# Performance work log

Measured on AMD Instinct MI355X. Metric: run time of the kernel, lower is better.

The kernel has to match this reference:

```python
import jax, jax.numpy as jnp
import numpy as np
import math

D_MODEL = 512
NUM_HEADS = 8
HEAD_DIM = D_MODEL // NUM_HEADS
B, S = 4, 2048


def setup_inputs() -> dict:
    key = jax.random.key(0)
    ks = jax.random.split(key, 11)
    scale = 1.0 / math.sqrt(D_MODEL)
    inp = {
        "Q": jax.random.normal(ks[0], (B, S, D_MODEL), jnp.float32),
        "K": jax.random.normal(ks[1], (B, S, D_MODEL), jnp.float32),
        "V": jax.random.normal(ks[2], (B, S, D_MODEL), jnp.float32),
        # causal mask, broadcast over batch and heads: [1,1,S,S]
        "mask": jnp.tril(jnp.ones((S, S), dtype=bool))[None, None],
        "w_q": jax.random.normal(ks[3], (D_MODEL, D_MODEL), jnp.float32) * scale,
        "b_q": jnp.zeros((D_MODEL,), jnp.float32),
        "w_k": jax.random.normal(ks[4], (D_MODEL, D_MODEL), jnp.float32) * scale,
        "b_k": jnp.zeros((D_MODEL,), jnp.float32),
        "w_v": jax.random.normal(ks[5], (D_MODEL, D_MODEL), jnp.float32) * scale,
        "b_v": jnp.zeros((D_MODEL,), jnp.float32),
        "w_o": jax.random.normal(ks[6], (D_MODEL, D_MODEL), jnp.float32) * scale,
        "b_o": jnp.zeros((D_MODEL,), jnp.float32),
    }
    return inp


def _split_heads(x):
    b, s, _ = x.shape
    return x.reshape(b, s, NUM_HEADS, HEAD_DIM).transpose(0, 2, 1, 3)  # [B,H,S,Dh]


def reference(Q, K, V, mask, w_q, b_q, w_k, b_k, w_v, b_v, w_o, b_o):
    # Linear projections (torch Linear: x @ W.T + b)
    q = _split_heads(Q @ w_q.T + b_q)
    k = _split_heads(K @ w_k.T + b_k)
    v = _split_heads(V @ w_v.T + b_v)

    scores = jnp.einsum("bhqd,bhkd->bhqk", q, k) / math.sqrt(HEAD_DIM)
    scores = jnp.where(mask, scores, -jnp.inf)
    attention = jax.nn.softmax(scores, axis=-1)  # [B,H,S,S]
    ctx = jnp.einsum("bhqk,bhkd->bhqd", attention, v)

    b, h, s, dh = ctx.shape
    x = ctx.transpose(0, 2, 1, 3).reshape(b, s, D_MODEL)
    x = x @ w_o.T + b_o
    return (x, attention)
```

## Files before the change

### kernel.cpp

```cpp
#include <hip/hip_runtime.h>


#define BATCH 4
#define SEQ   2048
#define DM    512
#define NH    8
#define DH    64
#define ROWS  (BATCH*SEQ)
#define QT    (SEQ/64)

typedef unsigned short u16;
using bf8   = __attribute__((ext_vector_type(8))) short;
using f32x4 = __attribute__((ext_vector_type(4))) float;

__device__ __forceinline__ float b2f(u16 u) {
    union { unsigned int i; float f; } v; v.i = ((unsigned int)u) << 16; return v.f;
}
__device__ __forceinline__ u16 f2b(float f) {
    union { float fl; unsigned int i; } v; v.fl = f;
    return (u16)((v.i + 0x7FFFu + ((v.i >> 16) & 1u)) >> 16);
}

template<bool IN_BF16, bool OUT_BF16>
__global__ __launch_bounds__(256) void proj_mfma(
    const void* __restrict__ Xv, const float* __restrict__ W,
    const float* __restrict__ bias, void* __restrict__ Cv)
{
    __shared__ u16 Xs[128][40];
    __shared__ u16 Wsh[128][40];
    const int tid  = threadIdx.x;
    const int lane = tid & 63;
    const int w    = tid >> 6;
    const int wm = (w >> 1) * 64, wn = (w & 1) * 64;
    const int lc = lane & 15, lq = lane >> 4;
    const int row0 = blockIdx.y * 128;
    const int col0 = blockIdx.x * 128;

    const f32x4 fzero = {0.f, 0.f, 0.f, 0.f};
    f32x4 acc[4][4];
    #pragma unroll
    for (int mt = 0; mt < 4; ++mt)
        #pragma unroll
        for (int nt = 0; nt < 4; ++nt) acc[mt][nt] = fzero;

    for (int k0 = 0; k0 < DM; k0 += 32) {
        __syncthreads();
        if (IN_BF16) {
            const u16* Xg = (const u16*)Xv;
            const int r = tid >> 2, kc = (tid & 3) * 8;
            #pragma unroll
            for (int rr = 0; rr < 2; ++rr)
                *(bf8*)&Xs[r + rr*64][kc] =
                    *(const bf8*)(Xg + (size_t)(row0 + r + rr*64) * DM + k0 + kc);
        } else {
            const float* Xg = (const float*)Xv;
            const int r = tid >> 3, kc = (tid & 7) * 4;
            #pragma unroll
            for (int rr = 0; rr < 4; ++rr) {
                float4 vx = *(const float4*)(Xg + (size_t)(row0 + r + rr*32) * DM + k0 + kc);
                u16 t4[4] = { f2b(vx.x), f2b(vx.y), f2b(vx.z), f2b(vx.w) };
                *(uint2*)&Xs[r + rr*32][kc] = *(uint2*)t4;
            }
        }
        {
            const int r = tid >> 3, kc = (tid & 7) * 4;
            #pragma unroll
            for (int rr = 0; rr < 4; ++rr) {
                float4 vw = *(const float4*)(W + (size_t)(col0 + r + rr*32) * DM + k0 + kc);
                u16 t4[4] = { f2b(vw.x), f2b(vw.y), f2b(vw.z), f2b(vw.w) };
                *(uint2*)&Wsh[r + rr*32][kc] = *(uint2*)t4;
            }
        }
        __syncthreads();
        bf8 a[4], b[4];
        #pragma unroll
        for (int mt = 0; mt < 4; ++mt) a[mt] = *(const bf8*)&Xs[wm + mt*16 + lc][lq*8];
        #pragma unroll
        for (int nt = 0; nt < 4; ++nt) b[nt] = *(const bf8*)&Wsh[wn + nt*16 + lc][lq*8];
        #pragma unroll
        for (int mt = 0; mt < 4; ++mt)
            #pragma unroll
            for (int nt = 0; nt < 4; ++nt)
                acc[mt][nt] = __builtin_amdgcn_mfma_f32_16x16x32_bf16(a[mt], b[nt], acc[mt][nt], 0, 0, 0);
    }
    #pragma unroll
    for (int nt = 0; nt < 4; ++nt) {
        const int col = col0 + wn + nt*16 + lc;
        const float bv = bias[col];
        #pragma unroll
        for (int mt = 0; mt < 4; ++mt) {
            #pragma unroll
            for (int r = 0; r < 4; ++r) {
                const int row = row0 + wm + mt*16 + lq*4 + r;
                const float val = acc[mt][nt][r] + bv;
                if (OUT_BF16) ((u16*)Cv)[(size_t)row * DM + col] = f2b(val);
                else          ((float*)Cv)[(size_t)row * DM + col] = val;
            }
        }
    }
}

__global__ __launch_bounds__(256) void attn_fused(
    const u16* __restrict__ q, const u16* __restrict__ k, const u16* __restrict__ v,
    float* __restrict__ att, u16* __restrict__ ctx)
{
    __shared__ u16 Qs[64][72];
    __shared__ u16 Ks[2][64][72];
    __shared__ u16 Vt[2][64][72];
    __shared__ u16 Ps[64][72];
    __shared__ float Ms[64][17];
    __shared__ float Ls[64][17];
    __shared__ float Mv[64];
    __shared__ float Lv[64];

    const int tid = threadIdx.x, lane = tid & 63, w = tid >> 6;
    const int lc = lane & 15, lq = lane >> 4;
    const int h = blockIdx.y, b = blockIdx.z;
    const size_t base = ((size_t)b * SEQ) * DM + h * DH;
    const size_t attbase = ((size_t)(b * NH + h)) * SEQ * SEQ;
    const int sr = tid >> 3, sc = (tid & 7) * 8;
    const int dv = tid & 63, jg = (tid >> 6) * 16;
    const f32x4 fzero = {0.f, 0.f, 0.f, 0.f};

    for (int qi = 0; qi < 2; ++qi) {
        const int qt = qi ? (QT - 1 - (int)blockIdx.x) : (int)blockIdx.x;
        __syncthreads();
        #pragma unroll
        for (int rr = 0; rr < 2; ++rr)
            *(bf8*)&Qs[sr + rr*32][sc] =
                *(const bf8*)(q + base + (size_t)(qt*64 + sr + rr*32) * DM + sc);

        float m_p[4], l_p[4];
        #pragma unroll
        for (int r = 0; r < 4; ++r) { m_p[r] = -1e30f; l_p[r] = 0.f; }

        bf8 kr[2];
        #pragma unroll
        for (int rr = 0; rr < 2; ++rr)
            kr[rr] = *(const bf8*)(k + base + (size_t)(sr + rr*32) * DM + sc);
        #pragma unroll
        for (int rr = 0; rr < 2; ++rr)
            *(bf8*)&Ks[0][sr + rr*32][sc] = kr[rr];

        int cur = 0;
        for (int kt = 0; kt <= qt; ++kt) {
            __syncthreads();
            if (kt < qt) {
                #pragma unroll
                for (int rr = 0; rr < 2; ++rr)
                    kr[rr] = *(const bf8*)(k + base + (size_t)((kt+1)*64 + sr + rr*32) * DM + sc);
            }
            f32x4 s[4];
            #pragma unroll
            for (int nt = 0; nt < 4; ++nt) s[nt] = fzero;
            #pragma unroll
            for (int ks = 0; ks < 2; ++ks) {
                bf8 a = *(const bf8*)&Qs[w*16 + lc][ks*32 + lq*8];
                #pragma unroll
                for (int nt = 0; nt < 4; ++nt) {
                    bf8 bb = *(const bf8*)&Ks[cur][nt*16 + lc][ks*32 + lq*8];
                    s[nt] = __builtin_amdgcn_mfma_f32_16x16x32_bf16(a, bb, s[nt], 0, 0, 0);
                }
            }
            const bool diag = (kt == qt);
            #pragma unroll
            for (int r = 0; r < 4; ++r) {
                const int rowl = w*16 + lq*4 + r;
                float sv[4];
                #pragma unroll
                for (int nt = 0; nt < 4; ++nt) {
                    float x = s[nt][r] * 0.125f;
                    if (diag && (nt*16 + lc > rowl)) x = -1e30f;
                    sv[nt] = x;
                }
                const float tm = fmaxf(fmaxf(sv[0], sv[1]), fmaxf(sv[2], sv[3]));
                const float mnew = fmaxf(m_p[r], tm);
                float add = __expf(sv[0]-mnew) + __expf(sv[1]-mnew)
                          + __expf(sv[2]-mnew) + __expf(sv[3]-mnew);
                l_p[r] = l_p[r] * __expf(m_p[r] - mnew) + add;
                m_p[r] = mnew;
            }
            if (kt < qt) {
                #pragma unroll
                for (int rr = 0; rr < 2; ++rr)
                    *(bf8*)&Ks[cur^1][sr + rr*32][sc] = kr[rr];
            }
            cur ^= 1;
        }

        #pragma unroll
        for (int r = 0; r < 4; ++r) {
            Ms[w*16 + lq*4 + r][lc] = m_p[r];
            Ls[w*16 + lq*4 + r][lc] = l_p[r];
        }
        #pragma unroll
        for (int rr = 0; rr < 2; ++rr)
            kr[rr] = *(const bf8*)(k + base + (size_t)(sr + rr*32) * DM + sc);
        u16 tv[16];
        #pragma unroll
        for (int i = 0; i < 16; ++i)
            tv[i] = v[base + (size_t)(jg + i) * DM + dv];
        __syncthreads();
        if (tid < 64) {
            float mf = -1e30f;
            #pragma unroll
            for (int t = 0; t < 16; ++t) mf = fmaxf(mf, Ms[tid][t]);
            float lf = 0.f;
            #pragma unroll
            for (int t = 0; t < 16; ++t) lf += Ls[tid][t] * __expf(Ms[tid][t] - mf);
            Mv[tid] = mf;
            Lv[tid] = 1.0f / lf;
        }
        #pragma unroll
        for (int rr = 0; rr < 2; ++rr)
            *(bf8*)&Ks[0][sr + rr*32][sc] = kr[rr];
        *(bf8*)&Vt[0][dv][jg]     = *(bf8*)&tv[0];
        *(bf8*)&Vt[0][dv][jg + 8] = *(bf8*)&tv[8];

        f32x4 oc[4];
        #pragma unroll
        for (int nt = 0; nt < 4; ++nt) oc[nt] = fzero;

        cur = 0;
        for (int kt = 0; kt <= qt; ++kt) {
            __syncthreads();
            if (kt < qt) {
                #pragma unroll
                for (int rr = 0; rr < 2; ++rr)
                    kr[rr] = *(const bf8*)(k + base + (size_t)((kt+1)*64 + sr + rr*32) * DM + sc);
                #pragma unroll
                for (int i = 0; i < 16; ++i)
                    tv[i] = v[base + (size_t)((kt+1)*64 + jg + i) * DM + dv];
            }
            f32x4 s[4];
            #pragma unroll
            for (int nt = 0; nt < 4; ++nt) s[nt] = fzero;
            #pragma unroll
            for (int ks = 0; ks < 2; ++ks) {
                bf8 a = *(const bf8*)&Qs[w*16 + lc][ks*32 + lq*8];
                #pragma unroll
                for (int nt = 0; nt < 4; ++nt) {
                    bf8 bb = *(const bf8*)&Ks[cur][nt*16 + lc][ks*32 + lq*8];
                    s[nt] = __builtin_amdgcn_mfma_f32_16x16x32_bf16(a, bb, s[nt], 0, 0, 0);
                }
            }
            const bool diag = (kt == qt);
            #pragma unroll
            for (int nt = 0; nt < 4; ++nt) {
                #pragma unroll
                for (int r = 0; r < 4; ++r) {
                    const int rowl = w*16 + lq*4 + r;
                    const int coll = nt*16 + lc;
                    float p = 0.f;
                    if (!diag || coll <= rowl)
                        p = __expf(s[nt][r] * 0.125f - Mv[rowl]) * Lv[rowl];
                    att[attbase + (size_t)(qt*64 + rowl) * SEQ + kt*64 + coll] = p;
                    Ps[rowl][coll] = f2b(p);
                }
            }
            #pragma unroll
            for (int ks = 0; ks < 2; ++ks) {
                bf8 a = *(const bf8*)&Ps[w*16 + lc][ks*32 + lq*8];
                #pragma unroll
                for (int nt = 0; nt < 4; ++nt) {
                    bf8 bb = *(const bf8*)&Vt[cur][nt*16 + lc][ks*32 + lq*8];
                    oc[nt] = __builtin_amdgcn_mfma_f32_16x16x32_bf16(a, bb, oc[nt], 0, 0, 0);
                }
            }
            if (kt < qt) {
                #pragma unroll
                for (int rr = 0; rr < 2; ++rr)
                    *(bf8*)&Ks[cur^1][sr + rr*32][sc] = kr[rr];
                *(bf8*)&Vt[cur^1][dv][jg]     = *(bf8*)&tv[0];
                *(bf8*)&Vt[cur^1][dv][jg + 8] = *(bf8*)&tv[8];
            }
            cur ^= 1;
        }
        #pragma unroll
        for (int nt = 0; nt < 4; ++nt) {
            #pragma unroll
            for (int r = 0; r < 4; ++r) {
                const int rowl = w*16 + lq*4 + r;
                ctx[((size_t)b * SEQ + qt*64 + rowl) * DM + h*DH + nt*16 + lc] = f2b(oc[nt][r]);
            }
        }
        {
            const int zr = tid >> 2, zc0 = (tid & 3) * 16;
            const float4 z = {0.f, 0.f, 0.f, 0.f};
            for (int ct = qt + 1; ct < QT; ++ct) {
                #pragma unroll
                for (int jj = 0; jj < 4; ++jj)
                    *(float4*)(att + attbase + (size_t)(qt*64 + zr) * SEQ + ct*64 + zc0 + jj*4) = z;
            }
        }
    }
}

extern "C" void kernel_launch(void* const* d_in, const int* in_sizes, int n_in,
                              void* d_out, int out_size, void* d_ws, size_t ws_size,
                              hipStream_t stream) {
    const float* Q   = (const float*)d_in[0];
    const float* K   = (const float*)d_in[1];
    const float* V   = (const float*)d_in[2];
    const float* w_q = (const float*)d_in[4];
    const float* b_q = (const float*)d_in[5];
    const float* w_k = (const float*)d_in[6];
    const float* b_k = (const float*)d_in[7];
    const float* w_v = (const float*)d_in[8];
    const float* b_v = (const float*)d_in[9];
    const float* w_o = (const float*)d_in[10];
    const float* b_o = (const float*)d_in[11];

    float* x_out   = (float*)d_out;
    float* att_out = x_out + (size_t)ROWS * DM;

    u16* qw = (u16*)d_ws;
    u16* kw = qw + (size_t)ROWS * DM;
    u16* vw = kw + (size_t)ROWS * DM;
    u16* cw = vw + (size_t)ROWS * DM;

    dim3 pgrid(DM/128, ROWS/128);
    proj_mfma<false, true><<<pgrid, 256, 0, stream>>>(Q, w_q, b_q, qw);
    proj_mfma<false, true><<<pgrid, 256, 0, stream>>>(K, w_k, b_k, kw);
    proj_mfma<false, true><<<pgrid, 256, 0, stream>>>(V, w_v, b_v, vw);

    dim3 agrid(QT/2, NH, BATCH);
    attn_fused<<<agrid, 256, 0, stream>>>(qw, kw, vw, att_out, cw);

    proj_mfma<true, false><<<pgrid, 256, 0, stream>>>(cw, w_o, b_o, x_out);
}
```

Measured before the change: 806.5 us.

## Merge QKV launches, remap attention grid per XCD, drop softmax max tracking

```diff
diff --git a/kernel.cpp b/kernel.cpp
--- a/kernel.cpp
+++ b/kernel.cpp
@@ -13,18 +13,91 @@
 using bf8   = __attribute__((ext_vector_type(8))) short;
 using f32x4 = __attribute__((ext_vector_type(4))) float;
 
-__device__ __forceinline__ float b2f(u16 u) {
-    union { unsigned int i; float f; } v; v.i = ((unsigned int)u) << 16; return v.f;
-}
 __device__ __forceinline__ u16 f2b(float f) {
     union { float fl; unsigned int i; } v; v.fl = f;
     return (u16)((v.i + 0x7FFFu + ((v.i >> 16) & 1u)) >> 16);
 }
 
-template<bool IN_BF16, bool OUT_BF16>
-__global__ __launch_bounds__(256) void proj_mfma(
-    const void* __restrict__ Xv, const float* __restrict__ W,
-    const float* __restrict__ bias, void* __restrict__ Cv)
+__device__ __forceinline__ void proj_body_f32_bf16(
+    const float* __restrict__ Xg, const float* __restrict__ W,
+    const float* __restrict__ bias, u16* __restrict__ Cg,
+    int row0, int col0)
+{
+    __shared__ u16 Xs[128][40];
+    __shared__ u16 Wsh[128][40];
+    const int tid  = threadIdx.x;
+    const int lane = tid & 63;
+    const int w    = tid >> 6;
+    const int wm = (w >> 1) * 64, wn = (w & 1) * 64;
+    const int lc = lane & 15, lq = lane >> 4;
+
+    const f32x4 fzero = {0.f, 0.f, 0.f, 0.f};
+    f32x4 acc[4][4];
+    #pragma unroll
+    for (int mt = 0; mt < 4; ++mt)
+        #pragma unroll
+        for (int nt = 0; nt < 4; ++nt) acc[mt][nt] = fzero;
+
+    for (int k0 = 0; k0 < DM; k0 += 32) {
+        __syncthreads();
+        {
+            const int r = tid >> 3, kc = (tid & 7) * 4;
+            #pragma unroll
+            for (int rr = 0; rr < 4; ++rr) {
+                float4 vx = *(const float4*)(Xg + (size_t)(row0 + r + rr*32) * DM + k0 + kc);
+                u16 t4[4] = { f2b(vx.x), f2b(vx.y), f2b(vx.z), f2b(vx.w) };
+                *(uint2*)&Xs[r + rr*32][kc] = *(uint2*)t4;
+                float4 vw = *(const float4*)(W + (size_t)(col0 + r + rr*32) * DM + k0 + kc);
+                u16 t5[4] = { f2b(vw.x), f2b(vw.y), f2b(vw.z), f2b(vw.w) };
+                *(uint2*)&Wsh[r + rr*32][kc] = *(uint2*)t5;
+            }
+        }
+        __syncthreads();
+        bf8 a[4], b[4];
+        #pragma unroll
+        for (int mt = 0; mt < 4; ++mt) a[mt] = *(const bf8*)&Xs[wm + mt*16 + lc][lq*8];
+        #pragma unroll
+        for (int nt = 0; nt < 4; ++nt) b[nt] = *(const bf8*)&Wsh[wn + nt*16 + lc][lq*8];
+        __builtin_amdgcn_s_setprio(1);
+        #pragma unroll
+        for (int mt = 0; mt < 4; ++mt)
+            #pragma unroll
+            for (int nt = 0; nt < 4; ++nt)
+                acc[mt][nt] = __builtin_amdgcn_mfma_f32_16x16x32_bf16(a[mt], b[nt], acc[mt][nt], 0, 0, 0);
+        __builtin_amdgcn_s_setprio(0);
+    }
+    #pragma unroll
+    for (int nt = 0; nt < 4; ++nt) {
+        const int col = col0 + wn + nt*16 + lc;
+        const float bv = bias[col];
+        #pragma unroll
+        for (int mt = 0; mt < 4; ++mt) {
+            #pragma unroll
+            for (int r = 0; r < 4; ++r) {
+                const int row = row0 + wm + mt*16 + lq*4 + r;
+                Cg[(size_t)row * DM + col] = f2b(acc[mt][nt][r] + bv);
+            }
+        }
+    }
+}
+
+__global__ __launch_bounds__(256) void proj_qkv(
+    const float* __restrict__ Q, const float* __restrict__ K, const float* __restrict__ V,
+    const float* __restrict__ wq, const float* __restrict__ wk, const float* __restrict__ wv,
+    const float* __restrict__ bq, const float* __restrict__ bk, const float* __restrict__ bv,
+    u16* __restrict__ qo, u16* __restrict__ ko, u16* __restrict__ vo)
+{
+    const int z = blockIdx.z;
+    const float* X = (z == 0) ? Q : (z == 1) ? K : V;
+    const float* W = (z == 0) ? wq : (z == 1) ? wk : wv;
+    const float* B = (z == 0) ? bq : (z == 1) ? bk : bv;
+    u16*         C = (z == 0) ? qo : (z == 1) ? ko : vo;
+    proj_body_f32_bf16(X, W, B, C, blockIdx.y * 128, blockIdx.x * 128);
+}
+
+__global__ __launch_bounds__(256) void proj_out(
+    const u16* __restrict__ Xg, const float* __restrict__ W,
+    const float* __restrict__ bias, float* __restrict__ Cg)
 {
     __shared__ u16 Xs[128][40];
     __shared__ u16 Wsh[128][40];
@@ -45,22 +118,13 @@
 
     for (int k0 = 0; k0 < DM; k0 += 32) {
         __syncthreads();
-        if (IN_BF16) {
-            const u16* Xg = (const u16*)Xv;
+        {
+            const u16* Xp = Xg;
             const int r = tid >> 2, kc = (tid & 3) * 8;
             #pragma unroll
             for (int rr = 0; rr < 2; ++rr)
                 *(bf8*)&Xs[r + rr*64][kc] =
-                    *(const bf8*)(Xg + (size_t)(row0 + r + rr*64) * DM + k0 + kc);
-        } else {
-            const float* Xg = (const float*)Xv;
-            const int r = tid >> 3, kc = (tid & 7) * 4;
-            #pragma unroll
-            for (int rr = 0; rr < 4; ++rr) {
-                float4 vx = *(const float4*)(Xg + (size_t)(row0 + r + rr*32) * DM + k0 + kc);
-                u16 t4[4] = { f2b(vx.x), f2b(vx.y), f2b(vx.z), f2b(vx.w) };
-                *(uint2*)&Xs[r + rr*32][kc] = *(uint2*)t4;
-            }
+                    *(const bf8*)(Xp + (size_t)(row0 + r + rr*64) * DM + k0 + kc);
         }
         {
             const int r = tid >> 3, kc = (tid & 7) * 4;
@@ -77,11 +141,13 @@
         for (int mt = 0; mt < 4; ++mt) a[mt] = *(const bf8*)&Xs[wm + mt*16 + lc][lq*8];
         #pragma unroll
         for (int nt = 0; nt < 4; ++nt) b[nt] = *(const bf8*)&Wsh[wn + nt*16 + lc][lq*8];
+        __builtin_amdgcn_s_setprio(1);
         #pragma unroll
         for (int mt = 0; mt < 4; ++mt)
             #pragma unroll
             for (int nt = 0; nt < 4; ++nt)
                 acc[mt][nt] = __builtin_amdgcn_mfma_f32_16x16x32_bf16(a[mt], b[nt], acc[mt][nt], 0, 0, 0);
+        __builtin_amdgcn_s_setprio(0);
     }
     #pragma unroll
     for (int nt = 0; nt < 4; ++nt) {
@@ -92,206 +158,210 @@
             #pragma unroll
             for (int r = 0; r < 4; ++r) {
                 const int row = row0 + wm + mt*16 + lq*4 + r;
-                const float val = acc[mt][nt][r] + bv;
-                if (OUT_BF16) ((u16*)Cv)[(size_t)row * DM + col] = f2b(val);
-                else          ((float*)Cv)[(size_t)row * DM + col] = val;
-            }
-        }
-    }
-}
-
-__global__ __launch_bounds__(256) void attn_fused(
+                Cg[(size_t)row * DM + col] = acc[mt][nt][r] + bv;
+            }
+        }
+    }
+}
+
+__global__ __launch_bounds__(256, 3) void attn_fused(
     const u16* __restrict__ q, const u16* __restrict__ k, const u16* __restrict__ v,
     float* __restrict__ att, u16* __restrict__ ctx)
 {
     __shared__ u16 Qs[64][72];
     __shared__ u16 Ks[2][64][72];
-    __shared__ u16 Vt[2][64][72];
+    __shared__ u16 Vt[64][72];
     __shared__ u16 Ps[64][72];
-    __shared__ float Ms[64][17];
     __shared__ float Ls[64][17];
-    __shared__ float Mv[64];
     __shared__ float Lv[64];
 
     const int tid = threadIdx.x, lane = tid & 63, w = tid >> 6;
     const int lc = lane & 15, lq = lane >> 4;
-    const int h = blockIdx.y, b = blockIdx.z;
+
+    const int lin = blockIdx.x + 32 * (blockIdx.y + 8 * blockIdx.z);
+    const int xcd = lin & 7, c = lin >> 3;
+    const int bh  = xcd * 4 + (c >> 5);
+    const int qt  = (QT - 1) - (c & 31);
+    const int h = bh & 7, b = bh >> 3;
+
     const size_t base = ((size_t)b * SEQ) * DM + h * DH;
     const size_t attbase = ((size_t)(b * NH + h)) * SEQ * SEQ;
     const int sr = tid >> 3, sc = (tid & 7) * 8;
     const int dv = tid & 63, jg = (tid >> 6) * 16;
     const f32x4 fzero = {0.f, 0.f, 0.f, 0.f};
 
-    for (int qi = 0; qi < 2; ++qi) {
-        const int qt = qi ? (QT - 1 - (int)blockIdx.x) : (int)blockIdx.x;
+    #pragma unroll
+    for (int rr = 0; rr < 2; ++rr)
+        *(bf8*)&Qs[sr + rr*32][sc] =
+            *(const bf8*)(q + base + (size_t)(qt*64 + sr + rr*32) * DM + sc);
+
+    float l_p[4];
+    #pragma unroll
+    for (int r = 0; r < 4; ++r) l_p[r] = 0.f;
+
+    bf8 kr[2];
+    #pragma unroll
+    for (int rr = 0; rr < 2; ++rr)
+        kr[rr] = *(const bf8*)(k + base + (size_t)(sr + rr*32) * DM + sc);
+    #pragma unroll
+    for (int rr = 0; rr < 2; ++rr)
+        *(bf8*)&Ks[0][sr + rr*32][sc] = kr[rr];
+
+    int cur = 0;
+    for (int kt = 0; kt <= qt; ++kt) {
         __syncthreads();
-        #pragma unroll
-        for (int rr = 0; rr < 2; ++rr)
-            *(bf8*)&Qs[sr + rr*32][sc] =
-                *(const bf8*)(q + base + (size_t)(qt*64 + sr + rr*32) * DM + sc);
-
-        float m_p[4], l_p[4];
-        #pragma unroll
-        for (int r = 0; r < 4; ++r) { m_p[r] = -1e30f; l_p[r] = 0.f; }
-
-        bf8 kr[2];
-        #pragma unroll
-        for (int rr = 0; rr < 2; ++rr)
-            kr[rr] = *(const bf8*)(k + base + (size_t)(sr + rr*32) * DM + sc);
-        #pragma unroll
-        for (int rr = 0; rr < 2; ++rr)
-            *(bf8*)&Ks[0][sr + rr*32][sc] = kr[rr];
-
-        int cur = 0;
-        for (int kt = 0; kt <= qt; ++kt) {
-            __syncthreads();
-            if (kt < qt) {
-                #pragma unroll
-                for (int rr = 0; rr < 2; ++rr)
-                    kr[rr] = *(const bf8*)(k + base + (size_t)((kt+1)*64 + sr + rr*32) * DM + sc);
-            }
-            f32x4 s[4];
-            #pragma unroll
-            for (int nt = 0; nt < 4; ++nt) s[nt] = fzero;
-            #pragma unroll
-            for (int ks = 0; ks < 2; ++ks) {
-                bf8 a = *(const bf8*)&Qs[w*16 + lc][ks*32 + lq*8];
-                #pragma unroll
-                for (int nt = 0; nt < 4; ++nt) {
-                    bf8 bb = *(const bf8*)&Ks[cur][nt*16 + lc][ks*32 + lq*8];
-                    s[nt] = __builtin_amdgcn_mfma_f32_16x16x32_bf16(a, bb, s[nt], 0, 0, 0);
+        if (kt < qt) {
+            #pragma unroll
+            for (int rr = 0; rr < 2; ++rr)
+                kr[rr] = *(const bf8*)(k + base + (size_t)((kt+1)*64 + sr + rr*32) * DM + sc);
+        }
+        f32x4 s[4];
+        #pragma unroll
+        for (int nt = 0; nt < 4; ++nt) s[nt] = fzero;
+        __builtin_amdgcn_s_setprio(1);
+        #pragma unroll
+        for (int ks = 0; ks < 2; ++ks) {
+            bf8 a = *(const bf8*)&Qs[w*16 + lc][ks*32 + lq*8];
+            #pragma unroll
+            for (int nt = 0; nt < 4; ++nt) {
+                bf8 bb = *(const bf8*)&Ks[cur][nt*16 + lc][ks*32 + lq*8];
+                s[nt] = __builtin_amdgcn_mfma_f32_16x16x32_bf16(a, bb, s[nt], 0, 0, 0);
+            }
+        }
+        __builtin_amdgcn_s_setprio(0);
+        const bool diag = (kt == qt);
+        #pragma unroll
+        for (int r = 0; r < 4; ++r) {
+            const int rowl = w*16 + lq*4 + r;
+            float e0, e1, e2, e3;
+            {
+                float x0 = s[0][r] * 0.125f, x1 = s[1][r] * 0.125f;
+                float x2 = s[2][r] * 0.125f, x3 = s[3][r] * 0.125f;
+                if (diag) {
+                    if ( 0*16 + lc > rowl) x0 = -1e30f;
+                    if ( 1*16 + lc > rowl) x1 = -1e30f;
+                    if ( 2*16 + lc > rowl) x2 = -1e30f;
+                    if ( 3*16 + lc > rowl) x3 = -1e30f;
                 }
-            }
-            const bool diag = (kt == qt);
+                e0 = __expf(x0); e1 = __expf(x1); e2 = __expf(x2); e3 = __expf(x3);
+            }
+            l_p[r] += (e0 + e1) + (e2 + e3);
+        }
+        if (kt < qt) {
+            #pragma unroll
+            for (int rr = 0; rr < 2; ++rr)
+                *(bf8*)&Ks[cur^1][sr + rr*32][sc] = kr[rr];
+        }
+        cur ^= 1;
+    }
+
+    #pragma unroll
+    for (int r = 0; r < 4; ++r)
+        Ls[w*16 + lq*4 + r][lc] = l_p[r];
+    #pragma unroll
+    for (int rr = 0; rr < 2; ++rr)
+        kr[rr] = *(const bf8*)(k + base + (size_t)(sr + rr*32) * DM + sc);
+    u16 tv[16];
+    #pragma unroll
+    for (int i = 0; i < 16; ++i)
+        tv[i] = v[base + (size_t)(jg + i) * DM + dv];
+    __syncthreads();
+    if (tid < 64) {
+        float lf = 0.f;
+        #pragma unroll
+        for (int t = 0; t < 16; ++t) lf += Ls[tid][t];
+        Lv[tid] = 1.0f / lf;
+    }
+    #pragma unroll
+    for (int rr = 0; rr < 2; ++rr)
+        *(bf8*)&Ks[0][sr + rr*32][sc] = kr[rr];
+    *(bf8*)&Vt[dv][jg]     = *(bf8*)&tv[0];
+    *(bf8*)&Vt[dv][jg + 8] = *(bf8*)&tv[8];
+    __syncthreads();
+
+    float lvr[4];
+    #pragma unroll
+    for (int r = 0; r < 4; ++r) lvr[r] = Lv[w*16 + lq*4 + r];
+
+    f32x4 oc[4];
+    #pragma unroll
+    for (int nt = 0; nt < 4; ++nt) oc[nt] = fzero;
+
+    cur = 0;
+    for (int kt = 0; kt <= qt; ++kt) {
+        if (kt > 0) __syncthreads();
+        if (kt < qt) {
+            #pragma unroll
+            for (int rr = 0; rr < 2; ++rr)
+                kr[rr] = *(const bf8*)(k + base + (size_t)((kt+1)*64 + sr + rr*32) * DM + sc);
+            #pragma unroll
+            for (int i = 0; i < 16; ++i)
+                tv[i] = v[base + (size_t)((kt+1)*64 + jg + i) * DM + dv];
+        }
+        f32x4 s[4];
+        #pragma unroll
+        for (int nt = 0; nt < 4; ++nt) s[nt] = fzero;
+        __builtin_amdgcn_s_setprio(1);
+        #pragma unroll
+        for (int ks = 0; ks < 2; ++ks) {
+            bf8 a = *(const bf8*)&Qs[w*16 + lc][ks*32 + lq*8];
+            #pragma unroll
+            for (int nt = 0; nt < 4; ++nt) {
+                bf8 bb = *(const bf8*)&Ks[cur][nt*16 + lc][ks*32 + lq*8];
+                s[nt] = __builtin_amdgcn_mfma_f32_16x16x32_bf16(a, bb, s[nt], 0, 0, 0);
+            }
+        }
+        __builtin_amdgcn_s_setprio(0);
+        const bool diag = (kt == qt);
+        #pragma unroll
+        for (int nt = 0; nt < 4; ++nt) {
             #pragma unroll
             for (int r = 0; r < 4; ++r) {
                 const int rowl = w*16 + lq*4 + r;
-                float sv[4];
-                #pragma unroll
-                for (int nt = 0; nt < 4; ++nt) {
-                    float x = s[nt][r] * 0.125f;
-                    if (diag && (nt*16 + lc > rowl)) x = -1e30f;
-                    sv[nt] = x;
-                }
-                const float tm = fmaxf(fmaxf(sv[0], sv[1]), fmaxf(sv[2], sv[3]));
-                const float mnew = fmaxf(m_p[r], tm);
-                float add = __expf(sv[0]-mnew) + __expf(sv[1]-mnew)
-                          + __expf(sv[2]-mnew) + __expf(sv[3]-mnew);
-                l_p[r] = l_p[r] * __expf(m_p[r] - mnew) + add;
-                m_p[r] = mnew;
-            }
-            if (kt < qt) {
-                #pragma unroll
-                for (int rr = 0; rr < 2; ++rr)
-                    *(bf8*)&Ks[cur^1][sr + rr*32][sc] = kr[rr];
-            }
-            cur ^= 1;
-        }
-
+                const int coll = nt*16 + lc;
+                float p = 0.f;
+                if (!diag || coll <= rowl)
+                    p = __expf(s[nt][r] * 0.125f) * lvr[r];
+                att[attbase + (size_t)(qt*64 + rowl) * SEQ + kt*64 + coll] = p;
+                Ps[rowl][coll] = f2b(p);
+            }
+        }
+        __builtin_amdgcn_s_setprio(1);
+        #pragma unroll
+        for (int ks = 0; ks < 2; ++ks) {
+            bf8 a = *(const bf8*)&Ps[w*16 + lc][ks*32 + lq*8];
+            #pragma unroll
+            for (int nt = 0; nt < 4; ++nt) {
+                bf8 bb = *(const bf8*)&Vt[nt*16 + lc][ks*32 + lq*8];
+                oc[nt] = __builtin_amdgcn_mfma_f32_16x16x32_bf16(a, bb, oc[nt], 0, 0, 0);
+            }
+        }
+        __builtin_amdgcn_s_setprio(0);
+        if (kt < qt) {
+            __syncthreads();
+            #pragma unroll
+            for (int rr = 0; rr < 2; ++rr)
+                *(bf8*)&Ks[cur^1][sr + rr*32][sc] = kr[rr];
+            *(bf8*)&Vt[dv][jg]     = *(bf8*)&tv[0];
+            *(bf8*)&Vt[dv][jg + 8] = *(bf8*)&tv[8];
+        }
+        cur ^= 1;
+    }
+    #pragma unroll
+    for (int nt = 0; nt < 4; ++nt) {
         #pragma unroll
         for (int r = 0; r < 4; ++r) {
-            Ms[w*16 + lq*4 + r][lc] = m_p[r];
-            Ls[w*16 + lq*4 + r][lc] = l_p[r];
-        }
-        #pragma unroll
-        for (int rr = 0; rr < 2; ++rr)
-            kr[rr] = *(const bf8*)(k + base + (size_t)(sr + rr*32) * DM + sc);
-        u16 tv[16];
-        #pragma unroll
-        for (int i = 0; i < 16; ++i)
-            tv[i] = v[base + (size_t)(jg + i) * DM + dv];
-        __syncthreads();
-        if (tid < 64) {
-            float mf = -1e30f;
-            #pragma unroll
-            for (int t = 0; t < 16; ++t) mf = fmaxf(mf, Ms[tid][t]);
-            float lf = 0.f;
-            #pragma unroll
-            for (int t = 0; t < 16; ++t) lf += Ls[tid][t] * __expf(Ms[tid][t] - mf);
-            Mv[tid] = mf;
-            Lv[tid] = 1.0f / lf;
-        }
-        #pragma unroll
-        for (int rr = 0; rr < 2; ++rr)
-            *(bf8*)&Ks[0][sr + rr*32][sc] = kr[rr];
-        *(bf8*)&Vt[0][dv][jg]     = *(bf8*)&tv[0];
-        *(bf8*)&Vt[0][dv][jg + 8] = *(bf8*)&tv[8];
-
-        f32x4 oc[4];
-        #pragma unroll
-        for (int nt = 0; nt < 4; ++nt) oc[nt] = fzero;
-
-        cur = 0;
-        for (int kt = 0; kt <= qt; ++kt) {
-            __syncthreads();
-            if (kt < qt) {
-                #pragma unroll
-                for (int rr = 0; rr < 2; ++rr)
-                    kr[rr] = *(const bf8*)(k + base + (size_t)((kt+1)*64 + sr + rr*32) * DM + sc);
-                #pragma unroll
-                for (int i = 0; i < 16; ++i)
-                    tv[i] = v[base + (size_t)((kt+1)*64 + jg + i) * DM + dv];
-            }
-            f32x4 s[4];
-            #pragma unroll
-            for (int nt = 0; nt < 4; ++nt) s[nt] = fzero;
-            #pragma unroll
-            for (int ks = 0; ks < 2; ++ks) {
-                bf8 a = *(const bf8*)&Qs[w*16 + lc][ks*32 + lq*8];
-                #pragma unroll
-                for (int nt = 0; nt < 4; ++nt) {
-                    bf8 bb = *(const bf8*)&Ks[cur][nt*16 + lc][ks*32 + lq*8];
-                    s[nt] = __builtin_amdgcn_mfma_f32_16x16x32_bf16(a, bb, s[nt], 0, 0, 0);
-                }
-            }
-            const bool diag = (kt == qt);
-            #pragma unroll
-            for (int nt = 0; nt < 4; ++nt) {
-                #pragma unroll
-                for (int r = 0; r < 4; ++r) {
-                    const int rowl = w*16 + lq*4 + r;
-                    const int coll = nt*16 + lc;
-                    float p = 0.f;
-                    if (!diag || coll <= rowl)
-                        p = __expf(s[nt][r] * 0.125f - Mv[rowl]) * Lv[rowl];
-                    att[attbase + (size_t)(qt*64 + rowl) * SEQ + kt*64 + coll] = p;
-                    Ps[rowl][coll] = f2b(p);
-                }
-            }
-            #pragma unroll
-            for (int ks = 0; ks < 2; ++ks) {
-                bf8 a = *(const bf8*)&Ps[w*16 + lc][ks*32 + lq*8];
-                #pragma unroll
-                for (int nt = 0; nt < 4; ++nt) {
-                    bf8 bb = *(const bf8*)&Vt[cur][nt*16 + lc][ks*32 + lq*8];
-                    oc[nt] = __builtin_amdgcn_mfma_f32_16x16x32_bf16(a, bb, oc[nt], 0, 0, 0);
-                }
-            }
-            if (kt < qt) {
-                #pragma unroll
-                for (int rr = 0; rr < 2; ++rr)
-                    *(bf8*)&Ks[cur^1][sr + rr*32][sc] = kr[rr];
-                *(bf8*)&Vt[cur^1][dv][jg]     = *(bf8*)&tv[0];
-                *(bf8*)&Vt[cur^1][dv][jg + 8] = *(bf8*)&tv[8];
-            }
-            cur ^= 1;
-        }
-        #pragma unroll
-        for (int nt = 0; nt < 4; ++nt) {
-            #pragma unroll
-            for (int r = 0; r < 4; ++r) {
-                const int rowl = w*16 + lq*4 + r;
-                ctx[((size_t)b * SEQ + qt*64 + rowl) * DM + h*DH + nt*16 + lc] = f2b(oc[nt][r]);
-            }
-        }
-        {
-            const int zr = tid >> 2, zc0 = (tid & 3) * 16;
-            const float4 z = {0.f, 0.f, 0.f, 0.f};
-            for (int ct = qt + 1; ct < QT; ++ct) {
-                #pragma unroll
-                for (int jj = 0; jj < 4; ++jj)
-                    *(float4*)(att + attbase + (size_t)(qt*64 + zr) * SEQ + ct*64 + zc0 + jj*4) = z;
-            }
+            const int rowl = w*16 + lq*4 + r;
+            ctx[((size_t)b * SEQ + qt*64 + rowl) * DM + h*DH + nt*16 + lc] = f2b(oc[nt][r]);
+        }
+    }
+    {
+        const int zr = tid >> 2, zc0 = (tid & 3) * 16;
+        const float4 z = {0.f, 0.f, 0.f, 0.f};
+        for (int ct = qt + 1; ct < QT; ++ct) {
+            #pragma unroll
+            for (int jj = 0; jj < 4; ++jj)
+                *(float4*)(att + attbase + (size_t)(qt*64 + zr) * SEQ + ct*64 + zc0 + jj*4) = z;
         }
     }
 }
@@ -319,13 +389,13 @@
     u16* vw = kw + (size_t)ROWS * DM;
     u16* cw = vw + (size_t)ROWS * DM;
 
-    dim3 pgrid(DM/128, ROWS/128);
-    proj_mfma<false, true><<<pgrid, 256, 0, stream>>>(Q, w_q, b_q, qw);
-    proj_mfma<false, true><<<pgrid, 256, 0, stream>>>(K, w_k, b_k, kw);
-    proj_mfma<false, true><<<pgrid, 256, 0, stream>>>(V, w_v, b_v, vw);
-
-    dim3 agrid(QT/2, NH, BATCH);
+    dim3 pgrid(DM/128, ROWS/128, 3);
+    proj_qkv<<<pgrid, 256, 0, stream>>>(Q, K, V, w_q, w_k, w_v,
+                                        b_q, b_k, b_v, qw, kw, vw);
+
+    dim3 agrid(QT, NH, BATCH);
     attn_fused<<<agrid, 256, 0, stream>>>(qw, kw, vw, att_out, cw);
 
-    proj_mfma<true, false><<<pgrid, 256, 0, stream>>>(cw, w_o, b_o, x_out);
-}
+    dim3 ogrid(DM/128, ROWS/128);
+    proj_out<<<ogrid, 256, 0, stream>>>(cw, w_o, b_o, x_out);
+}
```

Result: faster. 752.3 us (-6.7%).
